# Kernel tuning notes

Hardware: AMD Instinct MI355X
Metric: run time of the kernel (lower is better)

Reference implementation:

```python
import jax, jax.numpy as jnp
import numpy as np

NUM_RAYS = 2048
NUM_SAMPLES = 128
HIDDEN = 256
NEAR, FAR = 2.0, 6.0


def setup_inputs() -> dict:
    key = jax.random.key(0)
    ks = jax.random.split(key, 8)
    positions = jax.random.normal(ks[0], (NUM_RAYS, NUM_SAMPLES, 3), jnp.float32)
    t = jax.random.uniform(ks[1], (NUM_RAYS, NUM_SAMPLES), jnp.float32)
    t_values = jnp.sort(NEAR + (FAR - NEAR) * t, axis=-1)  # monotonically increasing per ray
    def glorot(k, shape):
        fan_in, fan_out = shape
        s = jnp.sqrt(2.0 / (fan_in + fan_out))
        return jax.random.normal(k, shape, jnp.float32) * s
    return {
        "positions": positions,
        "t_values": t_values,
        "W0": glorot(ks[2], (3, HIDDEN)), "b0": jnp.zeros((HIDDEN,), jnp.float32),
        "W1": glorot(ks[3], (HIDDEN, HIDDEN)), "b1": jnp.zeros((HIDDEN,), jnp.float32),
        "W2": glorot(ks[4], (HIDDEN, HIDDEN)), "b2": jnp.zeros((HIDDEN,), jnp.float32),
        "W3": glorot(ks[5], (HIDDEN, 4)), "b3": jnp.zeros((4,), jnp.float32),
        "include_depth": 1,
    }


def _mlp(x, W0, b0, W1, b1, W2, b2, W3, b3):
    h = jax.nn.relu(x @ W0 + b0)
    h = jax.nn.relu(h @ W1 + b1)
    h = jax.nn.relu(h @ W2 + b2)
    return h @ W3 + b3  # (N, 4)


def _blend_weights(t_values, opacity):
    # t_values, opacity: (R, S)
    delta = t_values[:, 1:] - t_values[:, :-1]
    delta = jnp.concatenate([delta, jnp.full_like(delta[:, :1], 1e10)], axis=-1)
    alpha = 1.0 - jnp.exp(-(opacity * delta))
    trans = jnp.minimum(1.0, 1.0 - alpha + 1e-10)
    # drop last, prepend ones, then cumulative transmittance
    trans = jnp.concatenate([jnp.ones_like(trans[:, :1]), trans[:, :-1]], axis=-1)
    trans = jnp.cumprod(trans, axis=-1)
    return alpha * trans  # (R, S)


def reference(positions, t_values, W0, b0, W1, b1, W2, b2, W3, b3, include_depth):
    num_rays, num_samples = positions.shape[:2]
    pts = positions.reshape(-1, 3)
    color_o = _mlp(pts, W0, b0, W1, b1, W2, b2, W3, b3)
    color_o = color_o.reshape(num_rays, num_samples, 4)
    color = jax.nn.sigmoid(color_o[..., :3])           # (R, S, 3)
    opacity = jax.nn.softplus(color_o[..., 3])         # (R, S)
    weights = _blend_weights(t_values, opacity)        # (R, S)
    output_color = jnp.sum(weights[..., None] * color, axis=-2)  # (R, 3)
    w = weights[:, :-1]
    output_alpha = jnp.sum(w, axis=-1)                 # (R,)
    if include_depth:
        cutoff = jnp.argmax(w, axis=-1)
        # torch sets cutoff=-1 (last element) where alpha < 0.1
        cutoff = jnp.where(output_alpha < 0.1, num_samples - 1, cutoff)
        output_depth = t_values[jnp.arange(num_rays), cutoff]
        return output_color, output_alpha, output_depth
    return output_color, output_alpha
```

## Files before the change

### kernel.cpp

```cpp
#include <hip/hip_runtime.h>

#define NRAYS 2048
#define NSAMP 128
#define HID   256

typedef __attribute__((ext_vector_type(8))) _Float16 half8;
typedef __attribute__((ext_vector_type(4))) float f32x4;

__device__ __forceinline__ unsigned pack2(_Float16 a, _Float16 b){
  unsigned short ua = __builtin_bit_cast(unsigned short, a);
  unsigned short ub = __builtin_bit_cast(unsigned short, b);
  return (unsigned)ua | ((unsigned)ub << 16);
}

__global__ void prep_kernel(const float* __restrict__ W1,
                            const float* __restrict__ W2,
                            const float* __restrict__ W3,
                            _Float16* __restrict__ out)
{
  int idx = blockIdx.x * 256 + threadIdx.x;
  float v; int pk, base, lstep;
  if (idx < 65536){
    int k = idx >> 8, n = idx & 255;
    v = W1[idx] * 256.f; pk = (((k >> 3) << 8) + n) * 8 + (k & 7); base = 0; lstep = 65536;
  } else if (idx < 131072){
    int j = idx - 65536; int k = j >> 8, n = j & 255;
    v = W2[j] * 256.f; pk = (((k >> 3) << 8) + n) * 8 + (k & 7); base = 131072; lstep = 65536;
  } else if (idx < 135168){
    int j = idx - 131072;
    int n = (j >> 3) & 15;
    int k = ((j >> 7) << 3) | (j & 7);
    v = (n < 4) ? W3[k * 4 + n] * 256.f : 0.f; pk = j; base = 262144; lstep = 4096;
  } else return;
  _Float16 hi = (_Float16)v;
  _Float16 lo = (_Float16)(v - (float)hi);
  out[base + pk] = hi;
  out[base + lstep + pk] = lo;
}

__launch_bounds__(256, 2)
__global__ void nerf_kernel(const float* __restrict__ pos,
                            const float* __restrict__ tvals,
                            const float* __restrict__ W0,
                            const float* __restrict__ b0,
                            const float* __restrict__ b1,
                            const float* __restrict__ b2,
                            const float* __restrict__ b3,
                            const _Float16* __restrict__ wsu,
                            float* __restrict__ out)
{
  __shared__ __align__(16) _Float16 hbuf_hi[64 * HID];
  __shared__ __align__(16) _Float16 hbuf_lo[64 * HID];
  __shared__ float xls[NSAMP * 3];
  __shared__ float tl[NSAMP];
  __shared__ __align__(16) float obuf[NSAMP * 4];
  __shared__ float stot;
  __shared__ float redf[2][5];
  __shared__ int   redi[2];

  const int t    = threadIdx.x;
  const int ray  = blockIdx.x;
  const int lane = t & 63;
  const int wv   = t >> 6;
  const int ln   = lane & 15;
  const int hi   = lane >> 4;
  const int swzx = (ln & 7) << 4;
  const float USC = 1.f / 65536.f;

  {
    const float* pbase = pos + (size_t)ray * NSAMP * 3;
    xls[t] = pbase[t];
    if (t < NSAMP) xls[256 + t] = pbase[256 + t];
    if (t < NSAMP) tl[t] = tvals[(size_t)ray * NSAMP + t];
  }
  __syncthreads();

  const int c = (t & 127) << 1;
  const int lnb = ln * 512;

  for (int chunk = 0; chunk < 2; ++chunk){
    const int rbase = chunk << 6;

    {
      float wa0 = W0[c],       wb0 = W0[c + 1];
      float wa1 = W0[256 + c], wb1 = W0[256 + c + 1];
      float wa2 = W0[512 + c], wb2 = W0[512 + c + 1];
      float ba = b0[c], bb = b0[c + 1];
      int r0 = (t >> 7) << 5;
      for (int r = r0; r < r0 + 32; ++r){
        int gr = rbase + r;
        float x0 = xls[gr * 3 + 0], x1 = xls[gr * 3 + 1], x2 = xls[gr * 3 + 2];
        float ha = fmaxf(fmaf(x2, wa2, fmaf(x1, wa1, fmaf(x0, wa0, ba))), 0.f) * 256.f;
        float hb = fmaxf(fmaf(x2, wb2, fmaf(x1, wb1, fmaf(x0, wb0, bb))), 0.f) * 256.f;
        _Float16 ah = (_Float16)ha, bh = (_Float16)hb;
        _Float16 al = (_Float16)(ha - (float)ah), bl = (_Float16)(hb - (float)bh);
        int off = (r * 512 + c * 2) ^ ((r & 7) << 4);
        *(unsigned*)((char*)hbuf_hi + off) = pack2(ah, bh);
        *(unsigned*)((char*)hbuf_lo + off) = pack2(al, bl);
      }
    }
    __syncthreads();

    for (int L = 0; L < 2; ++L){
      const _Float16* Bhb = wsu + (L ? 131072 : 0);
      const _Float16* Blb = wsu + (L ? 196608 : 65536);
      const float* bias = L ? b2 : b1;
      const int n0 = wv * 64;

      f32x4 acc[4][4];
      #pragma unroll
      for (int mb = 0; mb < 4; ++mb)
        #pragma unroll
        for (int nb = 0; nb < 4; ++nb)
          acc[mb][nb] = 0.f;

      #pragma unroll 1
      for (int kk = 0; kk < 8; ++kk){
        const half8* Bhp = (const half8*)Bhb + (kk * 4 + hi) * 256 + n0 + ln;
        const half8* Blp = (const half8*)Blb + (kk * 4 + hi) * 256 + n0 + ln;
        half8 Bhf[4], Blf[4];
        #pragma unroll
        for (int nb = 0; nb < 4; ++nb){
          Bhf[nb] = Bhp[nb * 16];
          Blf[nb] = Blp[nb * 16];
        }
        int kx = lnb + ((kk * 64 + hi * 16) ^ swzx);
        #pragma unroll
        for (int mb = 0; mb < 4; ++mb){
          half8 Ahf = *(const half8*)((const char*)hbuf_hi + kx + mb * 8192);
          half8 Alf = *(const half8*)((const char*)hbuf_lo + kx + mb * 8192);
          #pragma unroll
          for (int nb = 0; nb < 4; ++nb)
            acc[mb][nb] = __builtin_amdgcn_mfma_f32_16x16x32_f16(Ahf, Bhf[nb], acc[mb][nb], 0, 0, 0);
          #pragma unroll
          for (int nb = 0; nb < 4; ++nb)
            acc[mb][nb] = __builtin_amdgcn_mfma_f32_16x16x32_f16(Ahf, Blf[nb], acc[mb][nb], 0, 0, 0);
          #pragma unroll
          for (int nb = 0; nb < 4; ++nb)
            acc[mb][nb] = __builtin_amdgcn_mfma_f32_16x16x32_f16(Alf, Bhf[nb], acc[mb][nb], 0, 0, 0);
        }
      }

      float bv[4];
      #pragma unroll
      for (int nb = 0; nb < 4; ++nb) bv[nb] = bias[n0 + nb * 16 + ln];

      __syncthreads();
      #pragma unroll
      for (int mb = 0; mb < 4; ++mb){
        #pragma unroll
        for (int nb = 0; nb < 4; ++nb){
          int col = n0 + nb * 16 + ln;
          #pragma unroll
          for (int r = 0; r < 4; ++r){
            int row = mb * 16 + hi * 4 + r;
            float f = fmaxf(fmaf(acc[mb][nb][r], USC, bv[nb]), 0.f) * 256.f;
            _Float16 fh = (_Float16)f;
            _Float16 fl = (_Float16)(f - (float)fh);
            int off = (row * 512 + col * 2) ^ ((row & 7) << 4);
            *(_Float16*)((char*)hbuf_hi + off) = fh;
            *(_Float16*)((char*)hbuf_lo + off) = fl;
          }
        }
      }
      __syncthreads();
    }

    {
      const _Float16* B3hb = wsu + 262144;
      const _Float16* B3lb = wsu + 266240;
      f32x4 a3 = 0.f;
      #pragma unroll 1
      for (int kk = 0; kk < 8; ++kk){
        int bi = (kk * 4 + hi) * 16 + ln;
        half8 Bhf = ((const half8*)B3hb)[bi];
        half8 Blf = ((const half8*)B3lb)[bi];
        int kx = lnb + ((kk * 64 + hi * 16) ^ swzx) + wv * 8192;
        half8 Ah = *(const half8*)((const char*)hbuf_hi + kx);
        half8 Al = *(const half8*)((const char*)hbuf_lo + kx);
        a3 = __builtin_amdgcn_mfma_f32_16x16x32_f16(Ah, Bhf, a3, 0, 0, 0);
        a3 = __builtin_amdgcn_mfma_f32_16x16x32_f16(Ah, Blf, a3, 0, 0, 0);
        a3 = __builtin_amdgcn_mfma_f32_16x16x32_f16(Al, Bhf, a3, 0, 0, 0);
      }
      if (ln < 4){
        float b3v = b3[ln];
        #pragma unroll
        for (int r = 0; r < 4; ++r){
          int row = rbase + wv * 16 + hi * 4 + r;
          obuf[row * 4 + ln] = fmaf(a3[r], USC, b3v);
        }
      }
    }
    __syncthreads();
  }

  float inc = 1.f, alpha = 0.f, sig0 = 0.f, sig1 = 0.f, sig2 = 0.f;
  if (t < NSAMP){
    const float4* ov = (const float4*)obuf;
    float4 o = ov[t];
    sig0 = 1.f / (1.f + expf(-o.x));
    sig1 = 1.f / (1.f + expf(-o.y));
    sig2 = 1.f / (1.f + expf(-o.z));
    float op = (o.w > 20.f) ? o.w : log1pf(expf(o.w));
    float delta = (t < NSAMP - 1) ? (tl[t + 1] - tl[t]) : 1e10f;
    alpha = 1.f - expf(-op * delta);
    float u = fminf(1.f, 1.f - alpha + 1e-10f);
    inc = u;
    #pragma unroll
    for (int off = 1; off < 64; off <<= 1){
      float v = __shfl_up(inc, off);
      if (lane >= off) inc *= v;
    }
    if (wv == 0 && lane == 63) stot = inc;
  }
  __syncthreads();
  if (t < NSAMP){
    float ex = __shfl_up(inc, 1);
    if (lane == 0) ex = 1.f;
    if (wv == 1) ex *= stot;
    float wgt = alpha * ex;
    float sr = wgt * sig0, sg = wgt * sig1, sb = wgt * sig2;
    float aw = (t < NSAMP - 1) ? wgt : 0.f;
    float wm = (t < NSAMP - 1) ? wgt : -1e30f;
    float wmv = wm;
    #pragma unroll
    for (int off = 32; off; off >>= 1){
      sr += __shfl_xor(sr, off);
      sg += __shfl_xor(sg, off);
      sb += __shfl_xor(sb, off);
      aw += __shfl_xor(aw, off);
      wm = fmaxf(wm, __shfl_xor(wm, off));
    }
    unsigned long long bal = __ballot(wmv == wm);
    int fi = __ffsll(bal) - 1;
    if (lane == 0){
      redf[wv][0] = sr; redf[wv][1] = sg; redf[wv][2] = sb;
      redf[wv][3] = aw; redf[wv][4] = wm;
      redi[wv] = fi;
    }
  }
  __syncthreads();
  if (t == 0){
    float cr = redf[0][0] + redf[1][0];
    float cg = redf[0][1] + redf[1][1];
    float cb = redf[0][2] + redf[1][2];
    float asum = redf[0][3] + redf[1][3];
    int idx = (redf[1][4] > redf[0][4]) ? (64 + redi[1]) : redi[0];
    int cutoff = (asum < 0.1f) ? (NSAMP - 1) : idx;
    out[ray * 3 + 0] = cr;
    out[ray * 3 + 1] = cg;
    out[ray * 3 + 2] = cb;
    out[NRAYS * 3 + ray] = asum;
    out[NRAYS * 4 + ray] = tl[cutoff];
  }
}

extern "C" void kernel_launch(void* const* d_in, const int* in_sizes, int n_in,
                              void* d_out, int out_size, void* d_ws, size_t ws_size,
                              hipStream_t stream) {
  const float* pos = (const float*)d_in[0];
  const float* tv  = (const float*)d_in[1];
  const float* W0  = (const float*)d_in[2];
  const float* b0  = (const float*)d_in[3];
  const float* W1  = (const float*)d_in[4];
  const float* b1  = (const float*)d_in[5];
  const float* W2  = (const float*)d_in[6];
  const float* b2  = (const float*)d_in[7];
  const float* W3  = (const float*)d_in[8];
  const float* b3  = (const float*)d_in[9];
  _Float16* wsu = (_Float16*)d_ws;

  prep_kernel<<<528, 256, 0, stream>>>(W1, W2, W3, wsu);
  nerf_kernel<<<NRAYS, 256, 0, stream>>>(pos, tv, W0, b0, b1, b2, b3, wsu, (float*)d_out);
}
```

Measured before the change: 195.2 us.

## Software-pipeline B-fragment global loads across k iterations in MLP layers

Splits the four N-blocks of each k-step into two halves. The global loads for the next half (and the next k-step's first half) are issued before the MFMAs of the current half, so global-memory latency for the weight fragments overlaps with matrix work. It also reorders the MFMA chains so each accumulator gets its three split-precision products back to back, and reloads A fragments from LDS twice per k-step, using an asm barrier to keep the compiler from merging the loads. This adds LDS traffic and register pressure from the double-buffered B fragments.

```diff
diff --git a/kernel.cpp b/kernel.cpp
--- a/kernel.cpp
+++ b/kernel.cpp
@@ -102,8 +102,8 @@
     __syncthreads();
 
     for (int L = 0; L < 2; ++L){
-      const _Float16* Bhb = wsu + (L ? 131072 : 0);
-      const _Float16* Blb = wsu + (L ? 196608 : 65536);
+      const half8* Bh8 = (const half8*)(wsu + (L ? 131072 : 0));
+      const half8* Bl8 = (const half8*)(wsu + (L ? 196608 : 65536));
       const float* bias = L ? b2 : b1;
       const int n0 = wv * 64;
 
@@ -114,30 +114,52 @@
         for (int nb = 0; nb < 4; ++nb)
           acc[mb][nb] = 0.f;
 
+      half8 Ba_h[2], Ba_l[2], Bb_h[2], Bb_l[2];
+      {
+        int bi = hi * 256 + n0 + ln;
+        Ba_h[0] = Bh8[bi];      Ba_h[1] = Bh8[bi + 16];
+        Ba_l[0] = Bl8[bi];      Ba_l[1] = Bl8[bi + 16];
+      }
+
       #pragma unroll 1
       for (int kk = 0; kk < 8; ++kk){
-        const half8* Bhp = (const half8*)Bhb + (kk * 4 + hi) * 256 + n0 + ln;
-        const half8* Blp = (const half8*)Blb + (kk * 4 + hi) * 256 + n0 + ln;
-        half8 Bhf[4], Blf[4];
-        #pragma unroll
-        for (int nb = 0; nb < 4; ++nb){
-          Bhf[nb] = Bhp[nb * 16];
-          Blf[nb] = Blp[nb * 16];
-        }
-        int kx = lnb + ((kk * 64 + hi * 16) ^ swzx);
+        int kx  = lnb + ((kk * 64 + hi * 16) ^ swzx);
+        int bi0 = kk * 1024 + hi * 256 + n0 + ln;
+
+        {
+          int bi = bi0 + 32;
+          Bb_h[0] = Bh8[bi];  Bb_h[1] = Bh8[bi + 16];
+          Bb_l[0] = Bl8[bi];  Bb_l[1] = Bl8[bi + 16];
+        }
         #pragma unroll
         for (int mb = 0; mb < 4; ++mb){
           half8 Ahf = *(const half8*)((const char*)hbuf_hi + kx + mb * 8192);
           half8 Alf = *(const half8*)((const char*)hbuf_lo + kx + mb * 8192);
           #pragma unroll
-          for (int nb = 0; nb < 4; ++nb)
-            acc[mb][nb] = __builtin_amdgcn_mfma_f32_16x16x32_f16(Ahf, Bhf[nb], acc[mb][nb], 0, 0, 0);
+          for (int j = 0; j < 2; ++j){
+            acc[mb][j] = __builtin_amdgcn_mfma_f32_16x16x32_f16(Ahf, Ba_h[j], acc[mb][j], 0, 0, 0);
+            acc[mb][j] = __builtin_amdgcn_mfma_f32_16x16x32_f16(Ahf, Ba_l[j], acc[mb][j], 0, 0, 0);
+            acc[mb][j] = __builtin_amdgcn_mfma_f32_16x16x32_f16(Alf, Ba_h[j], acc[mb][j], 0, 0, 0);
+          }
+        }
+
+        if (kk < 7){
+          int bi = bi0 + 1024;
+          Ba_h[0] = Bh8[bi];  Ba_h[1] = Bh8[bi + 16];
+          Ba_l[0] = Bl8[bi];  Ba_l[1] = Bl8[bi + 16];
+        }
+        int kx2 = kx;
+        asm volatile("" : "+v"(kx2));
+        #pragma unroll
+        for (int mb = 0; mb < 4; ++mb){
+          half8 Ahf = *(const half8*)((const char*)hbuf_hi + kx2 + mb * 8192);
+          half8 Alf = *(const half8*)((const char*)hbuf_lo + kx2 + mb * 8192);
           #pragma unroll
-          for (int nb = 0; nb < 4; ++nb)
-            acc[mb][nb] = __builtin_amdgcn_mfma_f32_16x16x32_f16(Ahf, Blf[nb], acc[mb][nb], 0, 0, 0);
-          #pragma unroll
-          for (int nb = 0; nb < 4; ++nb)
-            acc[mb][nb] = __builtin_amdgcn_mfma_f32_16x16x32_f16(Alf, Bhf[nb], acc[mb][nb], 0, 0, 0);
+          for (int j = 0; j < 2; ++j){
+            acc[mb][2+j] = __builtin_amdgcn_mfma_f32_16x16x32_f16(Ahf, Bb_h[j], acc[mb][2+j], 0, 0, 0);
+            acc[mb][2+j] = __builtin_amdgcn_mfma_f32_16x16x32_f16(Ahf, Bb_l[j], acc[mb][2+j], 0, 0, 0);
+            acc[mb][2+j] = __builtin_amdgcn_mfma_f32_16x16x32_f16(Alf, Bb_h[j], acc[mb][2+j], 0, 0, 0);
+          }
         }
       }
 
```

After: 199.7 us. +2.3%, slower.

## Store activation low-part residual as 8-bit in LDS to cut shared memory

Applied to the files above, without the earlier changes.

The fp16 low-part residual of the split-precision activations is now rounded to an 8-bit encoding (the top byte of the fp16) and stored in a byte LDS buffer with its own swizzle. It is decoded back to half8 before the correction MFMA. This halves the LDS footprint of the low buffer, and launch bounds are raised to 3 blocks per CU to use the freed space for occupancy. In exchange it adds encode and decode ALU work, tightens the register budget, and loses precision in the residual term.

```diff
diff --git a/kernel.cpp b/kernel.cpp
--- a/kernel.cpp
+++ b/kernel.cpp
@@ -11,6 +11,21 @@
   unsigned short ua = __builtin_bit_cast(unsigned short, a);
   unsigned short ub = __builtin_bit_cast(unsigned short, b);
   return (unsigned)ua | ((unsigned)ub << 16);
+}
+
+__device__ __forceinline__ unsigned char enc8(_Float16 x){
+  unsigned short h = __builtin_bit_cast(unsigned short, x);
+  unsigned short r = (unsigned short)(h + 0x7F + ((h >> 8) & 1));
+  return (unsigned char)(r >> 8);
+}
+__device__ __forceinline__ half8 dec8(unsigned long long v){
+  half8 r;
+  #pragma unroll
+  for (int j = 0; j < 8; ++j){
+    unsigned short u = (unsigned short)(((v >> (8 * j)) & 0xFFull) << 8);
+    r[j] = __builtin_bit_cast(_Float16, u);
+  }
+  return r;
 }
 
 __global__ void prep_kernel(const float* __restrict__ W1,
@@ -38,7 +53,7 @@
   out[base + lstep + pk] = lo;
 }
 
-__launch_bounds__(256, 2)
+__launch_bounds__(256, 3)
 __global__ void nerf_kernel(const float* __restrict__ pos,
                             const float* __restrict__ tvals,
                             const float* __restrict__ W0,
@@ -49,8 +64,8 @@
                             const _Float16* __restrict__ wsu,
                             float* __restrict__ out)
 {
-  __shared__ __align__(16) _Float16 hbuf_hi[64 * HID];
-  __shared__ __align__(16) _Float16 hbuf_lo[64 * HID];
+  __shared__ __align__(16) _Float16      hbuf_hi[64 * HID];
+  __shared__ __align__(16) unsigned char hbuf_l8[64 * HID];
   __shared__ float xls[NSAMP * 3];
   __shared__ float tl[NSAMP];
   __shared__ __align__(16) float obuf[NSAMP * 4];
@@ -65,6 +80,7 @@
   const int ln   = lane & 15;
   const int hi   = lane >> 4;
   const int swzx = (ln & 7) << 4;
+  const int swz8 = (ln & 7) << 3;
   const float USC = 1.f / 65536.f;
 
   {
@@ -77,6 +93,7 @@
 
   const int c = (t & 127) << 1;
   const int lnb = ln * 512;
+  const int lnb8 = ln * 256;
 
   for (int chunk = 0; chunk < 2; ++chunk){
     const int rbase = chunk << 6;
@@ -94,16 +111,18 @@
         float hb = fmaxf(fmaf(x2, wb2, fmaf(x1, wb1, fmaf(x0, wb0, bb))), 0.f) * 256.f;
         _Float16 ah = (_Float16)ha, bh = (_Float16)hb;
         _Float16 al = (_Float16)(ha - (float)ah), bl = (_Float16)(hb - (float)bh);
-        int off = (r * 512 + c * 2) ^ ((r & 7) << 4);
-        *(unsigned*)((char*)hbuf_hi + off) = pack2(ah, bh);
-        *(unsigned*)((char*)hbuf_lo + off) = pack2(al, bl);
+        int offh = (r * 512 + c * 2) ^ ((r & 7) << 4);
+        *(unsigned*)((char*)hbuf_hi + offh) = pack2(ah, bh);
+        int off8 = r * 256 + (c ^ ((r & 7) << 3));
+        unsigned short lo2 = (unsigned short)enc8(al) | ((unsigned short)enc8(bl) << 8);
+        *(unsigned short*)(hbuf_l8 + off8) = lo2;
       }
     }
     __syncthreads();
 
     for (int L = 0; L < 2; ++L){
-      const _Float16* Bhb = wsu + (L ? 131072 : 0);
-      const _Float16* Blb = wsu + (L ? 196608 : 65536);
+      const half8* Bh8 = (const half8*)(wsu + (L ? 131072 : 0));
+      const half8* Bl8 = (const half8*)(wsu + (L ? 196608 : 65536));
       const float* bias = L ? b2 : b1;
       const int n0 = wv * 64;
 
@@ -116,19 +135,20 @@
 
       #pragma unroll 1
       for (int kk = 0; kk < 8; ++kk){
-        const half8* Bhp = (const half8*)Bhb + (kk * 4 + hi) * 256 + n0 + ln;
-        const half8* Blp = (const half8*)Blb + (kk * 4 + hi) * 256 + n0 + ln;
+        const half8* Bhp = Bh8 + (kk * 4 + hi) * 256 + n0 + ln;
+        const half8* Blp = Bl8 + (kk * 4 + hi) * 256 + n0 + ln;
         half8 Bhf[4], Blf[4];
         #pragma unroll
         for (int nb = 0; nb < 4; ++nb){
           Bhf[nb] = Bhp[nb * 16];
           Blf[nb] = Blp[nb * 16];
         }
-        int kx = lnb + ((kk * 64 + hi * 16) ^ swzx);
+        int kx  = lnb  + ((kk * 64 + hi * 16) ^ swzx);
+        int kx8 = lnb8 + ((kk * 32 + hi * 8)  ^ swz8);
         #pragma unroll
         for (int mb = 0; mb < 4; ++mb){
           half8 Ahf = *(const half8*)((const char*)hbuf_hi + kx + mb * 8192);
-          half8 Alf = *(const half8*)((const char*)hbuf_lo + kx + mb * 8192);
+          half8 Alf = dec8(*(const unsigned long long*)(hbuf_l8 + kx8 + mb * 4096));
           #pragma unroll
           for (int nb = 0; nb < 4; ++nb)
             acc[mb][nb] = __builtin_amdgcn_mfma_f32_16x16x32_f16(Ahf, Bhf[nb], acc[mb][nb], 0, 0, 0);
@@ -157,9 +177,10 @@
             float f = fmaxf(fmaf(acc[mb][nb][r], USC, bv[nb]), 0.f) * 256.f;
             _Float16 fh = (_Float16)f;
             _Float16 fl = (_Float16)(f - (float)fh);
-            int off = (row * 512 + col * 2) ^ ((row & 7) << 4);
-            *(_Float16*)((char*)hbuf_hi + off) = fh;
-            *(_Float16*)((char*)hbuf_lo + off) = fl;
+            int offh = (row * 512 + col * 2) ^ ((row & 7) << 4);
+            *(_Float16*)((char*)hbuf_hi + offh) = fh;
+            int off8 = row * 256 + (col ^ ((row & 7) << 3));
+            hbuf_l8[off8] = enc8(fl);
           }
         }
       }
@@ -175,9 +196,10 @@
         int bi = (kk * 4 + hi) * 16 + ln;
         half8 Bhf = ((const half8*)B3hb)[bi];
         half8 Blf = ((const half8*)B3lb)[bi];
-        int kx = lnb + ((kk * 64 + hi * 16) ^ swzx) + wv * 8192;
+        int kx  = lnb  + ((kk * 64 + hi * 16) ^ swzx) + wv * 8192;
+        int kx8 = lnb8 + ((kk * 32 + hi * 8)  ^ swz8) + wv * 4096;
         half8 Ah = *(const half8*)((const char*)hbuf_hi + kx);
-        half8 Al = *(const half8*)((const char*)hbuf_lo + kx);
+        half8 Al = dec8(*(const unsigned long long*)(hbuf_l8 + kx8));
         a3 = __builtin_amdgcn_mfma_f32_16x16x32_f16(Ah, Bhf, a3, 0, 0, 0);
         a3 = __builtin_amdgcn_mfma_f32_16x16x32_f16(Ah, Blf, a3, 0, 0, 0);
         a3 = __builtin_amdgcn_mfma_f32_16x16x32_f16(Al, Bhf, a3, 0, 0, 0);
```

Result: slower. 465.7 us (+138.6%).

## Switch hidden-layer GEMMs to 32x32x16 MFMA tiles with 16-row LDS swizzle

Applied to the files above, without the earlier changes.

Replaces the 16x16x32 MFMA tiling of the two 256x256 hidden layers with 32x32x16 MFMA instructions, so each wave holds four 32x32 accumulators instead of sixteen 16x16 ones. The LDS XOR swizzle widens from 8 to 16 rows to match the 32-row A-fragment access pattern, and the epilogue and final-layer loads are rewritten for the new layout. The aim is fewer instructions and less operand traffic per FLOP from larger MFMA tiles, at the cost of a more complex accumulator-to-row mapping.

```diff
diff --git a/kernel.cpp b/kernel.cpp
--- a/kernel.cpp
+++ b/kernel.cpp
@@ -6,6 +6,7 @@
 
 typedef __attribute__((ext_vector_type(8))) _Float16 half8;
 typedef __attribute__((ext_vector_type(4))) float f32x4;
+typedef __attribute__((ext_vector_type(16))) float f32x16;
 
 __device__ __forceinline__ unsigned pack2(_Float16 a, _Float16 b){
   unsigned short ua = __builtin_bit_cast(unsigned short, a);
@@ -64,7 +65,8 @@
   const int wv   = t >> 6;
   const int ln   = lane & 15;
   const int hi   = lane >> 4;
-  const int swzx = (ln & 7) << 4;
+  const int l31  = lane & 31;
+  const int kh   = lane >> 5;
   const float USC = 1.f / 65536.f;
 
   {
@@ -76,7 +78,6 @@
   __syncthreads();
 
   const int c = (t & 127) << 1;
-  const int lnb = ln * 512;
 
   for (int chunk = 0; chunk < 2; ++chunk){
     const int rbase = chunk << 6;
@@ -94,7 +95,7 @@
         float hb = fmaxf(fmaf(x2, wb2, fmaf(x1, wb1, fmaf(x0, wb0, bb))), 0.f) * 256.f;
         _Float16 ah = (_Float16)ha, bh = (_Float16)hb;
         _Float16 al = (_Float16)(ha - (float)ah), bl = (_Float16)(hb - (float)bh);
-        int off = (r * 512 + c * 2) ^ ((r & 7) << 4);
+        int off = (r * 512 + c * 2) ^ ((r & 15) << 4);
         *(unsigned*)((char*)hbuf_hi + off) = pack2(ah, bh);
         *(unsigned*)((char*)hbuf_lo + off) = pack2(al, bl);
       }
@@ -102,65 +103,64 @@
     __syncthreads();
 
     for (int L = 0; L < 2; ++L){
-      const _Float16* Bhb = wsu + (L ? 131072 : 0);
-      const _Float16* Blb = wsu + (L ? 196608 : 65536);
+      const half8* Bh8 = (const half8*)(wsu + (L ? 131072 : 0));
+      const half8* Bl8 = (const half8*)(wsu + (L ? 196608 : 65536));
       const float* bias = L ? b2 : b1;
       const int n0 = wv * 64;
-
-      f32x4 acc[4][4];
-      #pragma unroll
-      for (int mb = 0; mb < 4; ++mb)
-        #pragma unroll
-        for (int nb = 0; nb < 4; ++nb)
-          acc[mb][nb] = 0.f;
+      const int l31b = l31 * 512;
+      const int swz = (l31 & 15) << 4;
+
+      f32x16 acc00 = 0.f, acc01 = 0.f, acc10 = 0.f, acc11 = 0.f;
 
       #pragma unroll 1
-      for (int kk = 0; kk < 8; ++kk){
-        const half8* Bhp = (const half8*)Bhb + (kk * 4 + hi) * 256 + n0 + ln;
-        const half8* Blp = (const half8*)Blb + (kk * 4 + hi) * 256 + n0 + ln;
-        half8 Bhf[4], Blf[4];
-        #pragma unroll
-        for (int nb = 0; nb < 4; ++nb){
-          Bhf[nb] = Bhp[nb * 16];
-          Blf[nb] = Blp[nb * 16];
-        }
-        int kx = lnb + ((kk * 64 + hi * 16) ^ swzx);
-        #pragma unroll
-        for (int mb = 0; mb < 4; ++mb){
-          half8 Ahf = *(const half8*)((const char*)hbuf_hi + kx + mb * 8192);
-          half8 Alf = *(const half8*)((const char*)hbuf_lo + kx + mb * 8192);
-          #pragma unroll
-          for (int nb = 0; nb < 4; ++nb)
-            acc[mb][nb] = __builtin_amdgcn_mfma_f32_16x16x32_f16(Ahf, Bhf[nb], acc[mb][nb], 0, 0, 0);
-          #pragma unroll
-          for (int nb = 0; nb < 4; ++nb)
-            acc[mb][nb] = __builtin_amdgcn_mfma_f32_16x16x32_f16(Ahf, Blf[nb], acc[mb][nb], 0, 0, 0);
-          #pragma unroll
-          for (int nb = 0; nb < 4; ++nb)
-            acc[mb][nb] = __builtin_amdgcn_mfma_f32_16x16x32_f16(Alf, Bhf[nb], acc[mb][nb], 0, 0, 0);
-        }
-      }
-
-      float bv[4];
-      #pragma unroll
-      for (int nb = 0; nb < 4; ++nb) bv[nb] = bias[n0 + nb * 16 + ln];
+      for (int ks = 0; ks < 16; ++ks){
+        int bidx = (ks * 2 + kh) * 256 + n0 + l31;
+        half8 Bh0 = Bh8[bidx],      Bl0 = Bl8[bidx];
+        half8 Bh1 = Bh8[bidx + 32], Bl1 = Bl8[bidx + 32];
+        int off0 = l31b + ((ks * 32 + kh * 16) ^ swz);
+        {
+          half8 Ah = *(const half8*)((const char*)hbuf_hi + off0);
+          half8 Al = *(const half8*)((const char*)hbuf_lo + off0);
+          acc00 = __builtin_amdgcn_mfma_f32_32x32x16_f16(Ah, Bh0, acc00, 0, 0, 0);
+          acc00 = __builtin_amdgcn_mfma_f32_32x32x16_f16(Ah, Bl0, acc00, 0, 0, 0);
+          acc00 = __builtin_amdgcn_mfma_f32_32x32x16_f16(Al, Bh0, acc00, 0, 0, 0);
+          acc01 = __builtin_amdgcn_mfma_f32_32x32x16_f16(Ah, Bh1, acc01, 0, 0, 0);
+          acc01 = __builtin_amdgcn_mfma_f32_32x32x16_f16(Ah, Bl1, acc01, 0, 0, 0);
+          acc01 = __builtin_amdgcn_mfma_f32_32x32x16_f16(Al, Bh1, acc01, 0, 0, 0);
+        }
+        {
+          half8 Ah = *(const half8*)((const char*)hbuf_hi + off0 + 16384);
+          half8 Al = *(const half8*)((const char*)hbuf_lo + off0 + 16384);
+          acc10 = __builtin_amdgcn_mfma_f32_32x32x16_f16(Ah, Bh0, acc10, 0, 0, 0);
+          acc10 = __builtin_amdgcn_mfma_f32_32x32x16_f16(Ah, Bl0, acc10, 0, 0, 0);
+          acc10 = __builtin_amdgcn_mfma_f32_32x32x16_f16(Al, Bh0, acc10, 0, 0, 0);
+          acc11 = __builtin_amdgcn_mfma_f32_32x32x16_f16(Ah, Bh1, acc11, 0, 0, 0);
+          acc11 = __builtin_amdgcn_mfma_f32_32x32x16_f16(Ah, Bl1, acc11, 0, 0, 0);
+          acc11 = __builtin_amdgcn_mfma_f32_32x32x16_f16(Al, Bh1, acc11, 0, 0, 0);
+        }
+      }
+
+      float bv0 = bias[n0 + l31];
+      float bv1 = bias[n0 + 32 + l31];
 
       __syncthreads();
       #pragma unroll
-      for (int mb = 0; mb < 4; ++mb){
+      for (int i = 0; i < 16; ++i){
+        int rl = (i & 3) + ((i >> 2) << 3) + (kh << 2);
         #pragma unroll
-        for (int nb = 0; nb < 4; ++nb){
-          int col = n0 + nb * 16 + ln;
-          #pragma unroll
-          for (int r = 0; r < 4; ++r){
-            int row = mb * 16 + hi * 4 + r;
-            float f = fmaxf(fmaf(acc[mb][nb][r], USC, bv[nb]), 0.f) * 256.f;
-            _Float16 fh = (_Float16)f;
-            _Float16 fl = (_Float16)(f - (float)fh);
-            int off = (row * 512 + col * 2) ^ ((row & 7) << 4);
-            *(_Float16*)((char*)hbuf_hi + off) = fh;
-            *(_Float16*)((char*)hbuf_lo + off) = fl;
-          }
+        for (int tile = 0; tile < 4; ++tile){
+          int tr = tile >> 1, tc = tile & 1;
+          float v = (tile == 0) ? acc00[i] : (tile == 1) ? acc01[i]
+                   : (tile == 2) ? acc10[i] : acc11[i];
+          float bv = (tc == 0) ? bv0 : bv1;
+          int row = tr * 32 + rl;
+          int col = n0 + tc * 32 + l31;
+          float f = fmaxf(fmaf(v, USC, bv), 0.f) * 256.f;
+          _Float16 fh = (_Float16)f;
+          _Float16 fl = (_Float16)(f - (float)fh);
+          int off = (row * 512 + col * 2) ^ ((row & 15) << 4);
+          *(_Float16*)((char*)hbuf_hi + off) = fh;
+          *(_Float16*)((char*)hbuf_lo + off) = fl;
         }
       }
       __syncthreads();
@@ -170,14 +170,15 @@
       const _Float16* B3hb = wsu + 262144;
       const _Float16* B3lb = wsu + 266240;
       f32x4 a3 = 0.f;
+      const int row3 = wv * 16 + ln;
       #pragma unroll 1
       for (int kk = 0; kk < 8; ++kk){
         int bi = (kk * 4 + hi) * 16 + ln;
         half8 Bhf = ((const half8*)B3hb)[bi];
         half8 Blf = ((const half8*)B3lb)[bi];
-        int kx = lnb + ((kk * 64 + hi * 16) ^ swzx) + wv * 8192;
-        half8 Ah = *(const half8*)((const char*)hbuf_hi + kx);
-        half8 Al = *(const half8*)((const char*)hbuf_lo + kx);
+        int off = row3 * 512 + ((kk * 64 + hi * 16) ^ ((row3 & 15) << 4));
+        half8 Ah = *(const half8*)((const char*)hbuf_hi + off);
+        half8 Al = *(const half8*)((const char*)hbuf_lo + off);
         a3 = __builtin_amdgcn_mfma_f32_16x16x32_f16(Ah, Bhf, a3, 0, 0, 0);
         a3 = __builtin_amdgcn_mfma_f32_16x16x32_f16(Ah, Blf, a3, 0, 0, 0);
         a3 = __builtin_amdgcn_mfma_f32_16x16x32_f16(Al, Bhf, a3, 0, 0, 0);
```

Result: slower. 220.5 us (+12.9%).
